# Kernel optimization log

Measured on AMD Instinct MI355X. Metric: run time of the kernel, lower is better.

Reference implementation:

```python
import jax, jax.numpy as jnp
import numpy as np
import math

DT = 1024
HID = 512
B, M, N = 16, 1024, 1024
NEG_INF = -1.0e9


def _linear(x, w, b):
    # torch nn.Linear convention: w is (out, in)
    return x @ w.T + b


def setup_inputs() -> dict:
    key = jax.random.key(0)
    ks = jax.random.split(key, 20)
    s = 0.02
    inp = {
        "oV": jax.random.normal(ks[0], (B, M, DT), jnp.float32),
        "oT": jax.random.normal(ks[1], (B, N, DT), jnp.float32),
        "Wq_v_w": jax.random.normal(ks[2], (DT, DT), jnp.float32) * s,
        "Wq_v_b": jnp.zeros((DT,), jnp.float32),
        "Wk_t_w": jax.random.normal(ks[3], (DT, DT), jnp.float32) * s,
        "Wk_t_b": jnp.zeros((DT,), jnp.float32),
        "Wv_t_w": jax.random.normal(ks[4], (DT, DT), jnp.float32) * s,
        "Wv_t_b": jnp.zeros((DT,), jnp.float32),
        "Wq_t_w": jax.random.normal(ks[5], (DT, DT), jnp.float32) * s,
        "Wq_t_b": jnp.zeros((DT,), jnp.float32),
        "Wk_v_w": jax.random.normal(ks[6], (DT, DT), jnp.float32) * s,
        "Wk_v_b": jnp.zeros((DT,), jnp.float32),
        "Wv_v_w": jax.random.normal(ks[7], (DT, DT), jnp.float32) * s,
        "Wv_v_b": jnp.zeros((DT,), jnp.float32),
        "ffn1_w": jax.random.normal(ks[8], (HID, 2 * DT), jnp.float32) * s,
        "ffn1_b": jnp.zeros((HID,), jnp.float32),
        "ffn2_w": jax.random.normal(ks[9], (1, HID), jnp.float32) * s,
        "ffn2_b": jnp.zeros((1,), jnp.float32),
    }
    return inp


def reference(oV, oT, Wq_v_w, Wq_v_b, Wk_t_w, Wk_t_b, Wv_t_w, Wv_t_b,
              Wq_t_w, Wq_t_b, Wk_v_w, Wk_v_b, Wv_v_w, Wv_v_b,
              ffn1_w, ffn1_b, ffn2_w, ffn2_b):
    dt = oV.shape[-1]
    inv_sqrt = 1.0 / math.sqrt(dt)

    # shared similarity-derived mask
    sim_raw = jnp.einsum('bmd,bnd->bmn', oV, oT)            # (B, m, n)
    v_pool = oV.mean(axis=1)                                  # (B, dt)
    t_pool = oT.mean(axis=1)                                  # (B, dt)
    h = jax.nn.relu(_linear(jnp.concatenate([v_pool, t_pool], axis=-1), ffn1_w, ffn1_b))
    l = jax.nn.sigmoid(_linear(h, ffn2_w, ffn2_b))[:, 0]      # (B,)
    S = jax.nn.softmax(sim_raw * inv_sqrt, axis=-1)
    Mmask = S >= l[:, None, None]                             # (B, m, n) bool

    # V -> T masked cross-attention
    Q_v = _linear(oV, Wq_v_w, Wq_v_b)
    K_t = _linear(oT, Wk_t_w, Wk_t_b)
    V_t = _linear(oT, Wv_t_w, Wv_t_b)
    scores_vt = jnp.einsum('bmd,bnd->bmn', Q_v, K_t) * inv_sqrt
    attn_vt = jax.nn.softmax(jnp.where(Mmask, scores_vt, NEG_INF), axis=-1)
    out_vt = jnp.einsum('bmn,bnd->bmd', attn_vt, V_t)

    # T -> V masked cross-attention (transposed mask)
    Q_t = _linear(oT, Wq_t_w, Wq_t_b)
    K_v = _linear(oV, Wk_v_w, Wk_v_b)
    V_v = _linear(oV, Wv_v_w, Wv_v_b)
    scores_tv = jnp.einsum('bnd,bmd->bnm', Q_t, K_v) * inv_sqrt
    attn_tv = jax.nn.softmax(jnp.where(Mmask.transpose(0, 2, 1), scores_tv, NEG_INF), axis=-1)
    out_tv = jnp.einsum('bnm,bmd->bnd', attn_tv, V_v)

    return out_vt, out_tv, Mmask.astype(jnp.float32)
```

## Files before the change

### kernel.cpp

```cpp
#include <hip/hip_runtime.h>
#include <stdint.h>

typedef unsigned short u16;
typedef unsigned char  u8;
typedef unsigned int   u32;
typedef unsigned long long u64;
typedef __attribute__((ext_vector_type(8))) short  short8;
typedef __attribute__((ext_vector_type(4))) float  floatx4;

#define Bz   16
#define Mm   1024
#define Nn   1024
#define Dd   1024
#define HIDh 512
#define INV_SQRT_D 0.03125f
#define NEGINF (-1.0e9f)
#define BMDc  ((size_t)Bz * Mm * Dd)
#define sMDc  ((long)Mm * Dd)

__device__ __forceinline__ float bf2f(u16 h) {
    union { u32 u; float f; } c; c.u = ((u32)h) << 16; return c.f;
}
__device__ __forceinline__ u16 f2bf(float f) {
    union { float f; u32 u; } c; c.f = f;
    u32 u = c.u;
    return (u16)((u + 0x7FFFu + ((u >> 16) & 1u)) >> 16);
}
__device__ __forceinline__ void g2lds16(const u16* g, u16* l) {
    __builtin_amdgcn_global_load_lds((const __attribute__((address_space(1))) void*)g,
                                     (__attribute__((address_space(3))) void*)l, 16, 0, 0);
}

__device__ __forceinline__ float waveSum(float v) {
#pragma unroll
    for (int o = 32; o > 0; o >>= 1) v += __shfl_xor(v, o);
    return v;
}
__device__ __forceinline__ float waveMax(float v) {
#pragma unroll
    for (int o = 32; o > 0; o >>= 1) v = fmaxf(v, __shfl_xor(v, o));
    return v;
}

template <bool OUT_FP32>
__global__ __launch_bounds__(512, 2) void gemm256(
    const u16* __restrict__ A, const u16* __restrict__ Bm,
    void* __restrict__ Cv, int K, int ldc, long sA, long sB, long sC)
{
    __shared__ __align__(16) u16 lds[2][2][256 * 64];
    const int tid  = threadIdx.x;
    const int lane = tid & 63;
    const int wv   = tid >> 6;
    const int wr   = wv >> 2;
    const int wc   = wv & 3;
    const int fr   = lane & 15, fq = lane >> 4;

    const int gX = gridDim.x, gY = gridDim.y;
    int bid = blockIdx.x + gX * (blockIdx.y + gY * blockIdx.z);
    const int nwg = gX * gY * gridDim.z;
    int wg = (bid & 7) * (nwg >> 3) + (bid >> 3);
    const int bx = wg % gX; wg /= gX;
    const int by = wg % gY;
    const int bz = wg / gY;

    const long tileM = (long)bx * 256, tileN = (long)by * 256;
    A  += (long)bz * sA;
    Bm += (long)bz * sB;
    const int T = K >> 6;

    floatx4 acc[8][4];
#pragma unroll
    for (int i = 0; i < 8; ++i)
#pragma unroll
        for (int j = 0; j < 4; ++j) acc[i][j] = (floatx4){0.f, 0.f, 0.f, 0.f};

    const int lrow = lane >> 3;
    const int scol = ((lane & 7) ^ lrow) << 3;
    const int sw   = fr & 7;
    const int kc0  = ((fq ^ sw) << 3);
    const int kc1  = (((4 + fq) ^ sw) << 3);

    auto stage = [&](int tt, int side, int hh, int bb) {
#pragma unroll
        for (int i = 0; i < 2; ++i) {
            const int j = i * 8 + wv;
            const int prow = side ? (((j >> 2) << 6) + (hh << 5) + ((j & 3) << 3))
                                  : (((j >> 3) << 7) + (hh << 6) + ((j & 7) << 3));
            const u16* src = side ? Bm : A;
            const long rb  = side ? tileN : tileM;
            g2lds16(src + (size_t)(rb + prow + lrow) * (size_t)K + (size_t)(tt << 6) + scol,
                    &lds[bb][side][prow * 64]);
        }
    };

    short8 Af[4][2], Bf[4][2];
    auto quad = [&](int mb, int nb) {
#pragma unroll
        for (int m = 0; m < 4; ++m)
#pragma unroll
            for (int n = 0; n < 2; ++n) {
                acc[mb + m][nb + n] = __builtin_amdgcn_mfma_f32_16x16x32_bf16(
                    Af[m][0], Bf[nb + n][0], acc[mb + m][nb + n], 0, 0, 0);
                acc[mb + m][nb + n] = __builtin_amdgcn_mfma_f32_16x16x32_bf16(
                    Af[m][1], Bf[nb + n][1], acc[mb + m][nb + n], 0, 0, 0);
            }
    };

    stage(0, 0, 0, 0); stage(0, 1, 0, 0); stage(0, 1, 1, 0); stage(0, 0, 1, 0);
    stage(1, 0, 0, 1); stage(1, 1, 1, 1); stage(1, 0, 1, 1);
    asm volatile("s_waitcnt vmcnt(6)" ::: "memory");
    __builtin_amdgcn_s_barrier();

    for (int t = 0; t < T; ++t) {
        const int cb = t & 1;
        const u16* lA = &lds[cb][0][0];
        const u16* lB = &lds[cb][1][0];

#pragma unroll
        for (int m = 0; m < 4; ++m) {
            const int ro = ((wr << 7) + (m << 4) + fr) * 64;
            Af[m][0] = *(const short8*)&lA[ro + kc0];
            Af[m][1] = *(const short8*)&lA[ro + kc1];
        }
#pragma unroll
        for (int n = 0; n < 2; ++n) {
            const int ro = ((wc << 6) + (n << 4) + fr) * 64;
            Bf[n][0] = *(const short8*)&lB[ro + kc0];
            Bf[n][1] = *(const short8*)&lB[ro + kc1];
        }
        if (t + 1 < T) stage(t + 1, 1, 0, cb ^ 1);
        asm volatile("" ::: "memory");
        __builtin_amdgcn_s_barrier();
        asm volatile("s_waitcnt lgkmcnt(0)" ::: "memory");
        __builtin_amdgcn_sched_barrier(0);
        __builtin_amdgcn_s_setprio(1);
        quad(0, 0);
        __builtin_amdgcn_s_setprio(0);
        asm volatile("" ::: "memory");
        __builtin_amdgcn_s_barrier();

#pragma unroll
        for (int n = 2; n < 4; ++n) {
            const int ro = ((wc << 6) + (n << 4) + fr) * 64;
            Bf[n][0] = *(const short8*)&lB[ro + kc0];
            Bf[n][1] = *(const short8*)&lB[ro + kc1];
        }
        if (t + 2 < T) stage(t + 2, 0, 0, cb);
        asm volatile("" ::: "memory");
        __builtin_amdgcn_s_barrier();
        asm volatile("s_waitcnt lgkmcnt(0)" ::: "memory");
        __builtin_amdgcn_sched_barrier(0);
        __builtin_amdgcn_s_setprio(1);
        quad(0, 2);
        __builtin_amdgcn_s_setprio(0);
        asm volatile("" ::: "memory");
        __builtin_amdgcn_s_barrier();

#pragma unroll
        for (int m = 0; m < 4; ++m) {
            const int ro = ((wr << 7) + ((m + 4) << 4) + fr) * 64;
            Af[m][0] = *(const short8*)&lA[ro + kc0];
            Af[m][1] = *(const short8*)&lA[ro + kc1];
        }
        if (t + 2 < T) stage(t + 2, 1, 1, cb);
        asm volatile("" ::: "memory");
        __builtin_amdgcn_s_barrier();
        asm volatile("s_waitcnt lgkmcnt(0)" ::: "memory");
        __builtin_amdgcn_sched_barrier(0);
        __builtin_amdgcn_s_setprio(1);
        quad(4, 2);
        __builtin_amdgcn_s_setprio(0);
        asm volatile("" ::: "memory");
        __builtin_amdgcn_s_barrier();

        if (t + 2 < T) stage(t + 2, 0, 1, cb);
        asm volatile("" ::: "memory");
        __builtin_amdgcn_s_barrier();
        __builtin_amdgcn_s_setprio(1);
        quad(4, 0);
        __builtin_amdgcn_s_setprio(0);
        if (t + 1 < T) {
            if (t + 2 < T) asm volatile("s_waitcnt vmcnt(6)" ::: "memory");
            else           asm volatile("s_waitcnt vmcnt(0)" ::: "memory");
        }
        asm volatile("" ::: "memory");
        __builtin_amdgcn_s_barrier();
    }

    __syncthreads();
    if constexpr (!OUT_FP32) {
        u16* l2 = (u16*)&lds[0][0][0];
#pragma unroll
        for (int j = 0; j < 4; ++j) {
            const int col = (wc << 6) + (j << 4) + fr;
#pragma unroll
            for (int i = 0; i < 8; ++i) {
                const int row0 = (wr << 7) + (i << 4) + (fq << 2);
#pragma unroll
                for (int r = 0; r < 4; ++r)
                    l2[(row0 + r) * 256 + col] = f2bf(acc[i][j][r]);
            }
        }
        __syncthreads();
        u16* C = (u16*)Cv + (long)bz * sC;
#pragma unroll
        for (int it = 0; it < 16; ++it) {
            const int row = it * 16 + (tid >> 5);
            const int ch  = tid & 31;
            const short8 v = *(const short8*)&l2[row * 256 + ch * 8];
            *(short8*)&C[(tileM + row) * (long)ldc + tileN + ch * 8] = v;
        }
    } else {
        float* l2f = (float*)&lds[0][0][0];
        float* C = (float*)Cv + (long)bz * sC;
#pragma unroll
        for (int pass = 0; pass < 2; ++pass) {
            if (pass) __syncthreads();
            if (wr == pass) {
#pragma unroll
                for (int j = 0; j < 4; ++j) {
                    const int col = (wc << 6) + (j << 4) + fr;
#pragma unroll
                    for (int i = 0; i < 8; ++i) {
                        const int row0 = (i << 4) + (fq << 2);
#pragma unroll
                        for (int r = 0; r < 4; ++r)
                            l2f[(row0 + r) * 256 + col] = acc[i][j][r];
                    }
                }
            }
            __syncthreads();
#pragma unroll
            for (int it = 0; it < 16; ++it) {
                const int row = it * 8 + (tid >> 6);
                const int ch  = tid & 63;
                const float4 v = *(const float4*)&l2f[row * 256 + ch * 4];
                *(float4*)&C[(tileM + pass * 128 + row) * (long)ldc + tileN + ch * 4] = v;
            }
        }
    }
}

__global__ __launch_bounds__(512, 2) void gemm_proj3(
    const u16* __restrict__ A, const u16* __restrict__ Bm,
    const float* __restrict__ bcat,
    u16* __restrict__ Pq, u16* __restrict__ Pk, u16* __restrict__ Pv, int K)
{
    __shared__ __align__(16) u16 lds[2][2][256 * 64];
    const int tid  = threadIdx.x;
    const int lane = tid & 63;
    const int wv   = tid >> 6;
    const int wr   = wv >> 2;
    const int wc   = wv & 3;
    const int fr   = lane & 15, fq = lane >> 4;

    const int bid = blockIdx.x + 64 * blockIdx.y;
    const int x  = bid & 7, l = bid >> 3;
    const int x0 = (x & 3) * 16, y0 = (x >> 2) * 6;
    const int w = l >> 5, r = l & 31;
    int bx, by;
    if (w == 0)      { bx = x0 + (r & 7);      by = y0 + (r >> 3); }
    else if (w == 1) { bx = x0 + 8 + (r & 7);  by = y0 + (r >> 3); }
    else             { bx = x0 + (r & 15);     by = y0 + 4 + (r >> 4); }

    const long tileM = (long)bx * 256, tileN = (long)by * 256;
    const int T = K >> 6;

    floatx4 acc[8][4];
#pragma unroll
    for (int i = 0; i < 8; ++i)
#pragma unroll
        for (int j = 0; j < 4; ++j) acc[i][j] = (floatx4){0.f, 0.f, 0.f, 0.f};

    const int lrow = lane >> 3;
    const int scol = ((lane & 7) ^ lrow) << 3;
    const int sw   = fr & 7;
    const int kc0  = ((fq ^ sw) << 3);
    const int kc1  = (((4 + fq) ^ sw) << 3);

    auto stage = [&](int tt, int side, int hh, int bb) {
#pragma unroll
        for (int i = 0; i < 2; ++i) {
            const int j = i * 8 + wv;
            const int prow = side ? (((j >> 2) << 6) + (hh << 5) + ((j & 3) << 3))
                                  : (((j >> 3) << 7) + (hh << 6) + ((j & 7) << 3));
            const u16* src = side ? Bm : A;
            const long rb  = side ? tileN : tileM;
            g2lds16(src + (size_t)(rb + prow + lrow) * (size_t)K + (size_t)(tt << 6) + scol,
                    &lds[bb][side][prow * 64]);
        }
    };

    short8 Af[4][2], Bf[4][2];
    auto quad = [&](int mb, int nb) {
#pragma unroll
        for (int m = 0; m < 4; ++m)
#pragma unroll
            for (int n = 0; n < 2; ++n) {
                acc[mb + m][nb + n] = __builtin_amdgcn_mfma_f32_16x16x32_bf16(
                    Af[m][0], Bf[nb + n][0], acc[mb + m][nb + n], 0, 0, 0);
                acc[mb + m][nb + n] = __builtin_amdgcn_mfma_f32_16x16x32_bf16(
                    Af[m][1], Bf[nb + n][1], acc[mb + m][nb + n], 0, 0, 0);
            }
    };

    stage(0, 0, 0, 0); stage(0, 1, 0, 0); stage(0, 1, 1, 0); stage(0, 0, 1, 0);
    stage(1, 0, 0, 1); stage(1, 1, 1, 1); stage(1, 0, 1, 1);
    asm volatile("s_waitcnt vmcnt(6)" ::: "memory");
    __builtin_amdgcn_s_barrier();

    for (int t = 0; t < T; ++t) {
        const int cb = t & 1;
        const u16* lA = &lds[cb][0][0];
        const u16* lB = &lds[cb][1][0];

#pragma unroll
        for (int m = 0; m < 4; ++m) {
            const int ro = ((wr << 7) + (m << 4) + fr) * 64;
            Af[m][0] = *(const short8*)&lA[ro + kc0];
            Af[m][1] = *(const short8*)&lA[ro + kc1];
        }
#pragma unroll
        for (int n = 0; n < 2; ++n) {
            const int ro = ((wc << 6) + (n << 4) + fr) * 64;
            Bf[n][0] = *(const short8*)&lB[ro + kc0];
            Bf[n][1] = *(const short8*)&lB[ro + kc1];
        }
        if (t + 1 < T) stage(t + 1, 1, 0, cb ^ 1);
        asm volatile("" ::: "memory");
        __builtin_amdgcn_s_barrier();
        asm volatile("s_waitcnt lgkmcnt(0)" ::: "memory");
        __builtin_amdgcn_sched_barrier(0);
        __builtin_amdgcn_s_setprio(1);
        quad(0, 0);
        __builtin_amdgcn_s_setprio(0);
        asm volatile("" ::: "memory");
        __builtin_amdgcn_s_barrier();

#pragma unroll
        for (int n = 2; n < 4; ++n) {
            const int ro = ((wc << 6) + (n << 4) + fr) * 64;
            Bf[n][0] = *(const short8*)&lB[ro + kc0];
            Bf[n][1] = *(const short8*)&lB[ro + kc1];
        }
        if (t + 2 < T) stage(t + 2, 0, 0, cb);
        asm volatile("" ::: "memory");
        __builtin_amdgcn_s_barrier();
        asm volatile("s_waitcnt lgkmcnt(0)" ::: "memory");
        __builtin_amdgcn_sched_barrier(0);
        __builtin_amdgcn_s_setprio(1);
        quad(0, 2);
        __builtin_amdgcn_s_setprio(0);
        asm volatile("" ::: "memory");
        __builtin_amdgcn_s_barrier();

#pragma unroll
        for (int m = 0; m < 4; ++m) {
            const int ro = ((wr << 7) + ((m + 4) << 4) + fr) * 64;
            Af[m][0] = *(const short8*)&lA[ro + kc0];
            Af[m][1] = *(const short8*)&lA[ro + kc1];
        }
        if (t + 2 < T) stage(t + 2, 1, 1, cb);
        asm volatile("" ::: "memory");
        __builtin_amdgcn_s_barrier();
        asm volatile("s_waitcnt lgkmcnt(0)" ::: "memory");
        __builtin_amdgcn_sched_barrier(0);
        __builtin_amdgcn_s_setprio(1);
        quad(4, 2);
        __builtin_amdgcn_s_setprio(0);
        asm volatile("" ::: "memory");
        __builtin_amdgcn_s_barrier();

        if (t + 2 < T) stage(t + 2, 0, 1, cb);
        asm volatile("" ::: "memory");
        __builtin_amdgcn_s_barrier();
        __builtin_amdgcn_s_setprio(1);
        quad(4, 0);
        __builtin_amdgcn_s_setprio(0);
        if (t + 1 < T) {
            if (t + 2 < T) asm volatile("s_waitcnt vmcnt(6)" ::: "memory");
            else           asm volatile("s_waitcnt vmcnt(0)" ::: "memory");
        }
        asm volatile("" ::: "memory");
        __builtin_amdgcn_s_barrier();
    }

    const int oid = (int)(tileN >> 10);
    __syncthreads();
    if (oid < 2) {
        u16* l2 = (u16*)&lds[0][0][0];
#pragma unroll
        for (int j = 0; j < 4; ++j) {
            const int col = (wc << 6) + (j << 4) + fr;
            const float bv = bcat[tileN + col];
#pragma unroll
            for (int i = 0; i < 8; ++i) {
                const int row0 = (wr << 7) + (i << 4) + (fq << 2);
#pragma unroll
                for (int r = 0; r < 4; ++r)
                    l2[(row0 + r) * 256 + col] = f2bf(acc[i][j][r] + bv);
            }
        }
        __syncthreads();
        u16* P = oid ? Pk : Pq;
        const long colN = tileN & 1023;
#pragma unroll
        for (int it = 0; it < 16; ++it) {
            const int row = it * 16 + (tid >> 5);
            const int ch  = tid & 31;
            const short8 v = *(const short8*)&l2[row * 256 + ch * 8];
            *(short8*)&P[(tileM + row) * (long)Dd + colN + ch * 8] = v;
        }
    } else {
        char* l2c = (char*)&lds[0][0][0];
#pragma unroll
        for (int j = 0; j < 4; ++j) {
            const int col = (wc << 6) + (j << 4) + fr;
            const float bv = bcat[tileN + col];
            const int swz = (col & 7) << 4;
#pragma unroll
            for (int i = 0; i < 8; ++i) {
                const int row0 = (wr << 7) + (i << 4) + (fq << 2);
                const u64 pk = (u64)f2bf(acc[i][j][0] + bv)
                             | ((u64)f2bf(acc[i][j][1] + bv) << 16)
                             | ((u64)f2bf(acc[i][j][2] + bv) << 32)
                             | ((u64)f2bf(acc[i][j][3] + bv) << 48);
                *(u64*)(l2c + col * 512 + ((row0 * 2) ^ swz)) = pk;
            }
        }
        __syncthreads();
        const long b  = tileM >> 10, tm = tileM & 1023;
        const long colN = tileN & 1023;
#pragma unroll
        for (int it = 0; it < 16; ++it) {
            const int col = it * 16 + (tid >> 5);
            const int ch  = tid & 31;
            const short8 v = *(const short8*)(l2c + col * 512 + ((ch * 16) ^ ((col & 7) << 4)));
            *(short8*)&Pv[b * sMDc + (colN + col) * (long)Mm + tm + ch * 8] = v;
        }
    }
}

__global__ __launch_bounds__(256) void conv_pool(
    const float* __restrict__ oV, const float* __restrict__ oT,
    u16* __restrict__ oVb, u16* __restrict__ oTb,
    float* __restrict__ vpool, float* __restrict__ tpool)
{
    const int b = blockIdx.y, srci = blockIdx.z;
    const float* src = (srci ? oT : oV) + (size_t)b * Mm * Dd;
    u16* dst = (srci ? oTb : oVb) + (size_t)b * Mm * Dd;
    const int c4 = threadIdx.x * 4;
    const int r0 = blockIdx.x * 64;
    float4 s = {0.f, 0.f, 0.f, 0.f};
    for (int r = r0; r < r0 + 64; ++r) {
        const float4 v = *(const float4*)&src[(size_t)r * Dd + c4];
        s.x += v.x; s.y += v.y; s.z += v.z; s.w += v.w;
        ushort4 o;
        o.x = f2bf(v.x); o.y = f2bf(v.y); o.z = f2bf(v.z); o.w = f2bf(v.w);
        *(ushort4*)&dst[(size_t)r * Dd + c4] = o;
    }
    float* pool = (srci ? tpool : vpool) + (size_t)b * Dd + c4;
    atomicAdd(pool + 0, s.x * (1.0f / Mm));
    atomicAdd(pool + 1, s.y * (1.0f / Mm));
    atomicAdd(pool + 2, s.z * (1.0f / Mm));
    atomicAdd(pool + 3, s.w * (1.0f / Mm));
}

__global__ __launch_bounds__(256) void wconv6(
    const float* __restrict__ w0, const float* __restrict__ w1, const float* __restrict__ w2,
    const float* __restrict__ w3, const float* __restrict__ w4, const float* __restrict__ w5,
    u16* __restrict__ dst)
{
    const float* src;
    switch (blockIdx.y) {
        case 0: src = w0; break; case 1: src = w1; break; case 2: src = w2; break;
        case 3: src = w3; break; case 4: src = w4; break; default: src = w5; break;
    }
    const size_t i = (size_t)blockIdx.x * 256 + threadIdx.x;
    const float4 a = ((const float4*)src)[2 * i];
    const float4 b = ((const float4*)src)[2 * i + 1];
    short8 o;
    o[0]=(short)f2bf(a.x); o[1]=(short)f2bf(a.y); o[2]=(short)f2bf(a.z); o[3]=(short)f2bf(a.w);
    o[4]=(short)f2bf(b.x); o[5]=(short)f2bf(b.y); o[6]=(short)f2bf(b.z); o[7]=(short)f2bf(b.w);
    *(short8*)(dst + (((size_t)blockIdx.y) << 20) + 8 * i) = o;
}

__global__ __launch_bounds__(256) void bcat_kernel(
    const float* __restrict__ b0, const float* __restrict__ b1, const float* __restrict__ b2,
    const float* __restrict__ b3, const float* __restrict__ b4, const float* __restrict__ b5,
    float* __restrict__ out)
{
    const int i = blockIdx.x * 256 + threadIdx.x;
    const int seg = i >> 10;
    const float* s;
    switch (seg) {
        case 0: s = b0; break; case 1: s = b1; break; case 2: s = b2; break;
        case 3: s = b3; break; case 4: s = b4; break; default: s = b5; break;
    }
    out[i] = s[i & 1023];
}

__global__ __launch_bounds__(256) void ffn1_kernel(
    const float* __restrict__ vpool, const float* __restrict__ tpool,
    const float* __restrict__ f1w, const float* __restrict__ f1b,
    float* __restrict__ hbuf)
{
    const int j = blockIdx.x, b = blockIdx.y;
    const int t = threadIdx.x, wv = t >> 6, lane = t & 63;
    __shared__ float red[4];
    const float* w = f1w + (size_t)j * (2 * Dd);
    float a = 0.f;
    for (int k = t; k < Dd; k += 256) a += vpool[b * Dd + k] * w[k];
    for (int k = t; k < Dd; k += 256) a += tpool[b * Dd + k] * w[Dd + k];
    a = waveSum(a);
    if (lane == 0) red[wv] = a;
    __syncthreads();
    if (t == 0) hbuf[b * HIDh + j] = fmaxf(red[0] + red[1] + red[2] + red[3] + f1b[j], 0.0f);
}

__global__ __launch_bounds__(256) void ffn2_kernel(
    const float* __restrict__ hbuf, const float* __restrict__ f2w,
    const float* __restrict__ f2b, float* __restrict__ lbuf)
{
    const int b = blockIdx.x;
    const int t = threadIdx.x, wv = t >> 6, lane = t & 63;
    __shared__ float red[4];
    float p = 0.f;
    for (int j = t; j < HIDh; j += 256) p += hbuf[b * HIDh + j] * f2w[j];
    p = waveSum(p);
    if (lane == 0) red[wv] = p;
    __syncthreads();
    if (t == 0) {
        const float z = red[0] + red[1] + red[2] + red[3] + f2b[0];
        lbuf[b] = 1.0f / (1.0f + expf(-z));
    }
}

__global__ __launch_bounds__(256) void sim_softmax_mask(
    const u16* __restrict__ scores, const float* __restrict__ lbuf, float* __restrict__ maskF)
{
    const int row = blockIdx.x, b = blockIdx.y;
    const int t = threadIdx.x, wv = t >> 6, lane = t & 63;
    __shared__ float red[8];
    const size_t off = ((size_t)b * Mm + row) * Nn;
    const uint2 sv = *(const uint2*)(scores + off + 4 * t);
    const float x0 = bf2f((u16)(sv.x & 0xFFFFu)) * INV_SQRT_D;
    const float x1 = bf2f((u16)(sv.x >> 16))     * INV_SQRT_D;
    const float x2 = bf2f((u16)(sv.y & 0xFFFFu)) * INV_SQRT_D;
    const float x3 = bf2f((u16)(sv.y >> 16))     * INV_SQRT_D;
    float mx = waveMax(fmaxf(fmaxf(x0, x1), fmaxf(x2, x3)));
    if (lane == 0) red[wv] = mx;
    __syncthreads();
    mx = fmaxf(fmaxf(red[0], red[1]), fmaxf(red[2], red[3]));
    const float e0 = expf(x0 - mx), e1 = expf(x1 - mx), e2 = expf(x2 - mx), e3 = expf(x3 - mx);
    float s = waveSum(e0 + e1 + e2 + e3);
    if (lane == 0) red[4 + wv] = s;
    __syncthreads();
    const float inv = 1.0f / fmaxf(red[4] + red[5] + red[6] + red[7], 1e-30f);
    const float l = lbuf[b];
    float4 mk;
    mk.x = (e0 * inv >= l) ? 1.0f : 0.0f;
    mk.y = (e1 * inv >= l) ? 1.0f : 0.0f;
    mk.z = (e2 * inv >= l) ? 1.0f : 0.0f;
    mk.w = (e3 * inv >= l) ? 1.0f : 0.0f;
    *(float4*)(maskF + off + 4 * t) = mk;
}

__global__ __launch_bounds__(256) void transpose_mask(
    const float* __restrict__ maskF, u8* __restrict__ maskT)
{
    __shared__ u8 tile[64][68];
    const int m0 = blockIdx.x * 64, n0 = blockIdx.y * 64, b = blockIdx.z;
    const int t = threadIdx.x;
    const int r = t >> 2, c = (t & 3) * 16;
    const float* src = maskF + ((size_t)b * Mm + (m0 + r)) * Nn + n0 + c;
    float4 f0 = ((const float4*)src)[0];
    float4 f1 = ((const float4*)src)[1];
    float4 f2 = ((const float4*)src)[2];
    float4 f3 = ((const float4*)src)[3];
    u8* dst = &tile[r][c];
    dst[0]=f0.x!=0.f; dst[1]=f0.y!=0.f; dst[2]=f0.z!=0.f; dst[3]=f0.w!=0.f;
    dst[4]=f1.x!=0.f; dst[5]=f1.y!=0.f; dst[6]=f1.z!=0.f; dst[7]=f1.w!=0.f;
    dst[8]=f2.x!=0.f; dst[9]=f2.y!=0.f; dst[10]=f2.z!=0.f; dst[11]=f2.w!=0.f;
    dst[12]=f3.x!=0.f; dst[13]=f3.y!=0.f; dst[14]=f3.z!=0.f; dst[15]=f3.w!=0.f;
    __syncthreads();
    union { u8 b[16]; uint4 v; } pk;
#pragma unroll
    for (int k = 0; k < 16; ++k) pk.b[k] = tile[c + k][r];
    *(uint4*)(maskT + ((size_t)b * Nn + (n0 + r)) * Mm + m0 + c) = pk.v;
}

template <bool TRANSP>
__global__ __launch_bounds__(256) void masked_softmax(
    u16* __restrict__ scores, const float* __restrict__ maskF, const u8* __restrict__ maskT)
{
    const int row = blockIdx.x, b = blockIdx.y;
    const int t = threadIdx.x, wv = t >> 6, lane = t & 63;
    __shared__ float red[8];
    const size_t off = ((size_t)b * Mm + row) * Nn;
    const uint2 sv = *(const uint2*)(scores + off + 4 * t);
    float x0 = bf2f((u16)(sv.x & 0xFFFFu)) * INV_SQRT_D;
    float x1 = bf2f((u16)(sv.x >> 16))     * INV_SQRT_D;
    float x2 = bf2f((u16)(sv.y & 0xFFFFu)) * INV_SQRT_D;
    float x3 = bf2f((u16)(sv.y >> 16))     * INV_SQRT_D;
    if (TRANSP) {
        const u32 mk = *(const u32*)(maskT + off + 4 * t);
        if (!(mk & 0x000000FFu)) x0 = NEGINF;
        if (!(mk & 0x0000FF00u)) x1 = NEGINF;
        if (!(mk & 0x00FF0000u)) x2 = NEGINF;
        if (!(mk & 0xFF000000u)) x3 = NEGINF;
    } else {
        const float4 mk = *(const float4*)(maskF + off + 4 * t);
        if (mk.x == 0.f) x0 = NEGINF;
        if (mk.y == 0.f) x1 = NEGINF;
        if (mk.z == 0.f) x2 = NEGINF;
        if (mk.w == 0.f) x3 = NEGINF;
    }
    float mx = waveMax(fmaxf(fmaxf(x0, x1), fmaxf(x2, x3)));
    if (lane == 0) red[wv] = mx;
    __syncthreads();
    mx = fmaxf(fmaxf(red[0], red[1]), fmaxf(red[2], red[3]));
    const float e0 = expf(x0 - mx), e1 = expf(x1 - mx), e2 = expf(x2 - mx), e3 = expf(x3 - mx);
    float s = waveSum(e0 + e1 + e2 + e3);
    if (lane == 0) red[4 + wv] = s;
    __syncthreads();
    const float inv = 1.0f / fmaxf(red[4] + red[5] + red[6] + red[7], 1e-30f);
    uint2 pk;
    pk.x = (u32)f2bf(e0 * inv) | ((u32)f2bf(e1 * inv) << 16);
    pk.y = (u32)f2bf(e2 * inv) | ((u32)f2bf(e3 * inv) << 16);
    *(uint2*)(scores + off + 4 * t) = pk;
}

extern "C" void kernel_launch(void* const* d_in, const int* in_sizes, int n_in,
                              void* d_out, int out_size, void* d_ws, size_t ws_size,
                              hipStream_t stream)
{
    (void)in_sizes; (void)n_in; (void)out_size; (void)ws_size;
    const float* oV     = (const float*)d_in[0];
    const float* oT     = (const float*)d_in[1];
    const float* Wq_v_w = (const float*)d_in[2];
    const float* Wq_v_b = (const float*)d_in[3];
    const float* Wk_t_w = (const float*)d_in[4];
    const float* Wk_t_b = (const float*)d_in[5];
    const float* Wv_t_w = (const float*)d_in[6];
    const float* Wv_t_b = (const float*)d_in[7];
    const float* Wq_t_w = (const float*)d_in[8];
    const float* Wq_t_b = (const float*)d_in[9];
    const float* Wk_v_w = (const float*)d_in[10];
    const float* Wk_v_b = (const float*)d_in[11];
    const float* Wv_v_w = (const float*)d_in[12];
    const float* Wv_v_b = (const float*)d_in[13];
    const float* f1w    = (const float*)d_in[14];
    const float* f1b    = (const float*)d_in[15];
    const float* f2w    = (const float*)d_in[16];
    const float* f2b    = (const float*)d_in[17];

    float* out_vt = (float*)d_out;
    float* out_tv = out_vt + BMDc;
    float* maskF  = out_vt + 2 * BMDc;

    u16* S0a = (u16*)d_ws;
    u16* S1a = S0a + BMDc;
    u16* S2a = S1a + BMDc;
    u16* S0b = S2a + BMDc;
    u16* S1b = S0b + BMDc;
    u16* S2b = S1b + BMDc;
    u16* S3  = S2b + BMDc;
    u16* oVb = S3 + BMDc;
    u16* oTb = oVb + BMDc;
    u16* Wc  = oTb + BMDc;
    u8*  maskT = (u8*)(Wc + 6 * (1 << 20));
    float* bcat  = (float*)(maskT + BMDc);
    float* vpool = bcat + 6144;
    float* tpool = vpool + Bz * Dd;
    float* hbuf  = tpool + Bz * Dd;
    float* lbuf  = hbuf + Bz * HIDh;

    const dim3 blk(256), blk512(512);
    const dim3 gBat(Mm / 256, Nn / 256, Bz);
    const dim3 gFproj(64, 12, 1);
    const dim3 gRow(Mm, Bz);
    const dim3 gTrp(Mm / 64, Nn / 64, Bz);
    const long sMD = sMDc, sMN = (long)Mm * Nn;

    wconv6<<<dim3(512, 6), blk, 0, stream>>>(Wq_v_w, Wk_v_w, Wv_v_w, Wq_t_w, Wk_t_w, Wv_t_w, Wc);
    bcat_kernel<<<dim3(24), blk, 0, stream>>>(Wq_v_b, Wk_v_b, Wv_v_b, Wq_t_b, Wk_t_b, Wv_t_b, bcat);

    hipMemsetAsync(vpool, 0, 2 * Bz * Dd * sizeof(float), stream);
    conv_pool<<<dim3(16, Bz, 2), blk, 0, stream>>>(oV, oT, oVb, oTb, vpool, tpool);
    ffn1_kernel<<<dim3(HIDh, Bz), blk, 0, stream>>>(vpool, tpool, f1w, f1b, hbuf);
    ffn2_kernel<<<dim3(Bz), blk, 0, stream>>>(hbuf, f2w, f2b, lbuf);

    gemm256<false><<<gBat, blk512, 0, stream>>>(oVb, oTb, S3, Dd, Nn, sMD, sMD, sMN);
    sim_softmax_mask<<<gRow, blk, 0, stream>>>(S3, lbuf, maskF);
    transpose_mask<<<gTrp, blk, 0, stream>>>(maskF, maskT);

    gemm_proj3<<<gFproj, blk512, 0, stream>>>(oVb, Wc,                 bcat,        S0a, S1b, S2b, Dd);
    gemm_proj3<<<gFproj, blk512, 0, stream>>>(oTb, Wc + 3 * (1 << 20), bcat + 3072, S0b, S1a, S2a, Dd);

    gemm256<false><<<gBat, blk512, 0, stream>>>(S0a, S1a, S3, Dd, Nn, sMD, sMD, sMN);
    masked_softmax<false><<<gRow, blk, 0, stream>>>(S3, maskF, maskT);
    gemm256<true ><<<gBat, blk512, 0, stream>>>(S3, S2a, out_vt, Nn, Dd, sMN, sMD, sMD);

    gemm256<false><<<gBat, blk512, 0, stream>>>(S0b, S1b, S3, Dd, Nn, sMD, sMD, sMN);
    masked_softmax<true><<<gRow, blk, 0, stream>>>(S3, maskF, maskT);
    gemm256<true ><<<gBat, blk512, 0, stream>>>(S3, S2b, out_tv, Nn, Dd, sMN, sMD, sMD);
}
```

Before: 826.7 us.

## Batch paired GEMMs and softmaxes into single launches, swizzle epilogue LDS, use byte mask

```diff
diff --git a/kernel.cpp b/kernel.cpp
--- a/kernel.cpp
+++ b/kernel.cpp
@@ -44,8 +44,9 @@
 
 template <bool OUT_FP32>
 __global__ __launch_bounds__(512, 2) void gemm256(
-    const u16* __restrict__ A, const u16* __restrict__ Bm,
-    void* __restrict__ Cv, int K, int ldc, long sA, long sB, long sC)
+    const u16* __restrict__ Aa, const u16* __restrict__ Ba, void* __restrict__ Ca,
+    const u16* __restrict__ Ab, const u16* __restrict__ Bb, void* __restrict__ Cb,
+    int K, int ldc, long sA, long sB, long sC)
 {
     __shared__ __align__(16) u16 lds[2][2][256 * 64];
     const int tid  = threadIdx.x;
@@ -61,11 +62,15 @@
     int wg = (bid & 7) * (nwg >> 3) + (bid >> 3);
     const int bx = wg % gX; wg /= gX;
     const int by = wg % gY;
-    const int bz = wg / gY;
+    const int bz2 = wg / gY;
+    const int br = bz2 >> 4;
+    const int bz = bz2 & 15;
+
+    const u16* A  = (br ? Ab : Aa) + (long)bz * sA;
+    const u16* Bm = (br ? Bb : Ba) + (long)bz * sB;
+    void* Cv = br ? Cb : Ca;
 
     const long tileM = (long)bx * 256, tileN = (long)by * 256;
-    A  += (long)bz * sA;
-    Bm += (long)bz * sB;
     const int T = K >> 6;
 
     floatx4 acc[8][4];
@@ -193,12 +198,15 @@
 #pragma unroll
         for (int j = 0; j < 4; ++j) {
             const int col = (wc << 6) + (j << 4) + fr;
+            const int c   = col >> 3;
 #pragma unroll
             for (int i = 0; i < 8; ++i) {
                 const int row0 = (wr << 7) + (i << 4) + (fq << 2);
 #pragma unroll
-                for (int r = 0; r < 4; ++r)
-                    l2[(row0 + r) * 256 + col] = f2bf(acc[i][j][r]);
+                for (int r = 0; r < 4; ++r) {
+                    const int row = row0 + r;
+                    l2[row * 256 + (((c + row) & 31) << 3) + (col & 7)] = f2bf(acc[i][j][r]);
+                }
             }
         }
         __syncthreads();
@@ -207,7 +215,7 @@
         for (int it = 0; it < 16; ++it) {
             const int row = it * 16 + (tid >> 5);
             const int ch  = tid & 31;
-            const short8 v = *(const short8*)&l2[row * 256 + ch * 8];
+            const short8 v = *(const short8*)&l2[row * 256 + (((ch + row) & 31) << 3)];
             *(short8*)&C[(tileM + row) * (long)ldc + tileN + ch * 8] = v;
         }
     } else {
@@ -220,12 +228,13 @@
 #pragma unroll
                 for (int j = 0; j < 4; ++j) {
                     const int col = (wc << 6) + (j << 4) + fr;
+                    const int c   = col >> 2;
 #pragma unroll
                     for (int i = 0; i < 8; ++i) {
                         const int row0 = (i << 4) + (fq << 2);
 #pragma unroll
                         for (int r = 0; r < 4; ++r)
-                            l2f[(row0 + r) * 256 + col] = acc[i][j][r];
+                            l2f[(row0 + r) * 256 + (((c + (fq << 2)) & 63) << 2) + (col & 3)] = acc[i][j][r];
                     }
                 }
             }
@@ -234,7 +243,8 @@
             for (int it = 0; it < 16; ++it) {
                 const int row = it * 8 + (tid >> 6);
                 const int ch  = tid & 63;
-                const float4 v = *(const float4*)&l2f[row * 256 + ch * 4];
+                const int rot = (row >> 2) & 3;
+                const float4 v = *(const float4*)&l2f[row * 256 + (((ch + (rot << 2)) & 63) << 2)];
                 *(float4*)&C[(tileM + pass * 128 + row) * (long)ldc + tileN + ch * 4] = v;
             }
         }
@@ -242,9 +252,10 @@
 }
 
 __global__ __launch_bounds__(512, 2) void gemm_proj3(
-    const u16* __restrict__ A, const u16* __restrict__ Bm,
-    const float* __restrict__ bcat,
-    u16* __restrict__ Pq, u16* __restrict__ Pk, u16* __restrict__ Pv, int K)
+    const u16* __restrict__ A0, const u16* __restrict__ A1,
+    const u16* __restrict__ Wcat, const float* __restrict__ bc,
+    u16* __restrict__ Pq0, u16* __restrict__ Pk0, u16* __restrict__ Pv0,
+    u16* __restrict__ Pq1, u16* __restrict__ Pk1, u16* __restrict__ Pv1, int K)
 {
     __shared__ __align__(16) u16 lds[2][2][256 * 64];
     const int tid  = threadIdx.x;
@@ -253,6 +264,14 @@
     const int wr   = wv >> 2;
     const int wc   = wv & 3;
     const int fr   = lane & 15, fq = lane >> 4;
+
+    const int z = blockIdx.z;
+    const u16* A  = z ? A1 : A0;
+    const u16* Bm = Wcat + ((size_t)z * 3 * Dd * Dd);
+    const float* bcat = bc + z * 3072;
+    u16* Pq = z ? Pq1 : Pq0;
+    u16* Pk = z ? Pk1 : Pk0;
+    u16* Pv = z ? Pv1 : Pv0;
 
     const int bid = blockIdx.x + 64 * blockIdx.y;
     const int x  = bid & 7, l = bid >> 3;
@@ -392,13 +411,16 @@
 #pragma unroll
         for (int j = 0; j < 4; ++j) {
             const int col = (wc << 6) + (j << 4) + fr;
+            const int c   = col >> 3;
             const float bv = bcat[tileN + col];
 #pragma unroll
             for (int i = 0; i < 8; ++i) {
                 const int row0 = (wr << 7) + (i << 4) + (fq << 2);
 #pragma unroll
-                for (int r = 0; r < 4; ++r)
-                    l2[(row0 + r) * 256 + col] = f2bf(acc[i][j][r] + bv);
+                for (int r = 0; r < 4; ++r) {
+                    const int row = row0 + r;
+                    l2[row * 256 + (((c + row) & 31) << 3) + (col & 7)] = f2bf(acc[i][j][r] + bv);
+                }
             }
         }
         __syncthreads();
@@ -408,7 +430,7 @@
         for (int it = 0; it < 16; ++it) {
             const int row = it * 16 + (tid >> 5);
             const int ch  = tid & 31;
-            const short8 v = *(const short8*)&l2[row * 256 + ch * 8];
+            const short8 v = *(const short8*)&l2[row * 256 + (((ch + row) & 31) << 3)];
             *(short8*)&P[(tileM + row) * (long)Dd + colN + ch * 8] = v;
         }
     } else {
@@ -537,7 +559,8 @@
 }
 
 __global__ __launch_bounds__(256) void sim_softmax_mask(
-    const u16* __restrict__ scores, const float* __restrict__ lbuf, float* __restrict__ maskF)
+    const u16* __restrict__ scores, const float* __restrict__ lbuf,
+    float* __restrict__ maskF, u8* __restrict__ maskR)
 {
     const int row = blockIdx.x, b = blockIdx.y;
     const int t = threadIdx.x, wv = t >> 6, lane = t & 63;
@@ -564,25 +587,20 @@
     mk.z = (e2 * inv >= l) ? 1.0f : 0.0f;
     mk.w = (e3 * inv >= l) ? 1.0f : 0.0f;
     *(float4*)(maskF + off + 4 * t) = mk;
+    const u32 u8mk = (mk.x != 0.f ? 1u : 0u) | (mk.y != 0.f ? 0x100u : 0u)
+                   | (mk.z != 0.f ? 0x10000u : 0u) | (mk.w != 0.f ? 0x1000000u : 0u);
+    *(u32*)(maskR + off + 4 * t) = u8mk;
 }
 
 __global__ __launch_bounds__(256) void transpose_mask(
-    const float* __restrict__ maskF, u8* __restrict__ maskT)
+    const u8* __restrict__ maskR, u8* __restrict__ maskT)
 {
     __shared__ u8 tile[64][68];
     const int m0 = blockIdx.x * 64, n0 = blockIdx.y * 64, b = blockIdx.z;
     const int t = threadIdx.x;
     const int r = t >> 2, c = (t & 3) * 16;
-    const float* src = maskF + ((size_t)b * Mm + (m0 + r)) * Nn + n0 + c;
-    float4 f0 = ((const float4*)src)[0];
-    float4 f1 = ((const float4*)src)[1];
-    float4 f2 = ((const float4*)src)[2];
-    float4 f3 = ((const float4*)src)[3];
-    u8* dst = &tile[r][c];
-    dst[0]=f0.x!=0.f; dst[1]=f0.y!=0.f; dst[2]=f0.z!=0.f; dst[3]=f0.w!=0.f;
-    dst[4]=f1.x!=0.f; dst[5]=f1.y!=0.f; dst[6]=f1.z!=0.f; dst[7]=f1.w!=0.f;
-    dst[8]=f2.x!=0.f; dst[9]=f2.y!=0.f; dst[10]=f2.z!=0.f; dst[11]=f2.w!=0.f;
-    dst[12]=f3.x!=0.f; dst[13]=f3.y!=0.f; dst[14]=f3.z!=0.f; dst[15]=f3.w!=0.f;
+    const uint4 src = *(const uint4*)(maskR + ((size_t)b * Mm + (m0 + r)) * Nn + n0 + c);
+    *(uint4*)&tile[r][c] = src;
     __syncthreads();
     union { u8 b[16]; uint4 v; } pk;
 #pragma unroll
@@ -590,11 +608,14 @@
     *(uint4*)(maskT + ((size_t)b * Nn + (n0 + r)) * Mm + m0 + c) = pk.v;
 }
 
-template <bool TRANSP>
-__global__ __launch_bounds__(256) void masked_softmax(
-    u16* __restrict__ scores, const float* __restrict__ maskF, const u8* __restrict__ maskT)
-{
-    const int row = blockIdx.x, b = blockIdx.y;
+__global__ __launch_bounds__(256) void masked_softmax2(
+    u16* __restrict__ Sa, u16* __restrict__ Sb,
+    const u8* __restrict__ mR, const u8* __restrict__ mT)
+{
+    const int row = blockIdx.x, bb = blockIdx.y;
+    const int br = bb >> 4, b = bb & 15;
+    u16* scores = br ? Sb : Sa;
+    const u8* mask = br ? mT : mR;
     const int t = threadIdx.x, wv = t >> 6, lane = t & 63;
     __shared__ float red[8];
     const size_t off = ((size_t)b * Mm + row) * Nn;
@@ -603,19 +624,11 @@
     float x1 = bf2f((u16)(sv.x >> 16))     * INV_SQRT_D;
     float x2 = bf2f((u16)(sv.y & 0xFFFFu)) * INV_SQRT_D;
     float x3 = bf2f((u16)(sv.y >> 16))     * INV_SQRT_D;
-    if (TRANSP) {
-        const u32 mk = *(const u32*)(maskT + off + 4 * t);
-        if (!(mk & 0x000000FFu)) x0 = NEGINF;
-        if (!(mk & 0x0000FF00u)) x1 = NEGINF;
-        if (!(mk & 0x00FF0000u)) x2 = NEGINF;
-        if (!(mk & 0xFF000000u)) x3 = NEGINF;
-    } else {
-        const float4 mk = *(const float4*)(maskF + off + 4 * t);
-        if (mk.x == 0.f) x0 = NEGINF;
-        if (mk.y == 0.f) x1 = NEGINF;
-        if (mk.z == 0.f) x2 = NEGINF;
-        if (mk.w == 0.f) x3 = NEGINF;
-    }
+    const u32 mk = *(const u32*)(mask + off + 4 * t);
+    if (!(mk & 0x000000FFu)) x0 = NEGINF;
+    if (!(mk & 0x0000FF00u)) x1 = NEGINF;
+    if (!(mk & 0x00FF0000u)) x2 = NEGINF;
+    if (!(mk & 0xFF000000u)) x3 = NEGINF;
     float mx = waveMax(fmaxf(fmaxf(x0, x1), fmaxf(x2, x3)));
     if (lane == 0) red[wv] = mx;
     __syncthreads();
@@ -665,12 +678,14 @@
     u16* S0b = S2a + BMDc;
     u16* S1b = S0b + BMDc;
     u16* S2b = S1b + BMDc;
-    u16* S3  = S2b + BMDc;
-    u16* oVb = S3 + BMDc;
+    u16* S3a = S2b + BMDc;
+    u16* S3b = S3a + BMDc;
+    u16* oVb = S3b + BMDc;
     u16* oTb = oVb + BMDc;
     u16* Wc  = oTb + BMDc;
     u8*  maskT = (u8*)(Wc + 6 * (1 << 20));
-    float* bcat  = (float*)(maskT + BMDc);
+    u8*  maskR = maskT + BMDc;
+    float* bcat  = (float*)(maskR + BMDc);
     float* vpool = bcat + 6144;
     float* tpool = vpool + Bz * Dd;
     float* hbuf  = tpool + Bz * Dd;
@@ -678,8 +693,9 @@
 
     const dim3 blk(256), blk512(512);
     const dim3 gBat(Mm / 256, Nn / 256, Bz);
-    const dim3 gFproj(64, 12, 1);
-    const dim3 gRow(Mm, Bz);
+    const dim3 gBat2(Mm / 256, Nn / 256, 2 * Bz);
+    const dim3 gFproj(64, 12, 2);
+    const dim3 gRow2(Mm, 2 * Bz);
     const dim3 gTrp(Mm / 64, Nn / 64, Bz);
     const long sMD = sMDc, sMN = (long)Mm * Nn;
 
@@ -691,18 +707,16 @@
     ffn1_kernel<<<dim3(HIDh, Bz), blk, 0, stream>>>(vpool, tpool, f1w, f1b, hbuf);
     ffn2_kernel<<<dim3(Bz), blk, 0, stream>>>(hbuf, f2w, f2b, lbuf);
 
-    gemm256<false><<<gBat, blk512, 0, stream>>>(oVb, oTb, S3, Dd, Nn, sMD, sMD, sMN);
-    sim_softmax_mask<<<gRow, blk, 0, stream>>>(S3, lbuf, maskF);
-    transpose_mask<<<gTrp, blk, 0, stream>>>(maskF, maskT);
-
-    gemm_proj3<<<gFproj, blk512, 0, stream>>>(oVb, Wc,                 bcat,        S0a, S1b, S2b, Dd);
-    gemm_proj3<<<gFproj, blk512, 0, stream>>>(oTb, Wc + 3 * (1 << 20), bcat + 3072, S0b, S1a, S2a, Dd);
-
-    gemm256<false><<<gBat, blk512, 0, stream>>>(S0a, S1a, S3, Dd, Nn, sMD, sMD, sMN);
-    masked_softmax<false><<<gRow, blk, 0, stream>>>(S3, maskF, maskT);
-    gemm256<true ><<<gBat, blk512, 0, stream>>>(S3, S2a, out_vt, Nn, Dd, sMN, sMD, sMD);
-
-    gemm256<false><<<gBat, blk512, 0, stream>>>(S0b, S1b, S3, Dd, Nn, sMD, sMD, sMN);
-    masked_softmax<true><<<gRow, blk, 0, stream>>>(S3, maskF, maskT);
-    gemm256<true ><<<gBat, blk512, 0, stream>>>(S3, S2b, out_tv, Nn, Dd, sMN, sMD, sMD);
-}
+    gemm256<false><<<gBat, blk512, 0, stream>>>(oVb, oTb, S3a, oVb, oTb, S3a, Dd, Nn, sMD, sMD, sMN);
+    sim_softmax_mask<<<dim3(Mm, Bz), blk, 0, stream>>>(S3a, lbuf, maskF, maskR);
+    transpose_mask<<<gTrp, blk, 0, stream>>>(maskR, maskT);
+
+    gemm_proj3<<<gFproj, blk512, 0, stream>>>(oVb, oTb, Wc, bcat,
+                                              S0a, S1b, S2b, S0b, S1a, S2a, Dd);
+
+    gemm256<false><<<gBat2, blk512, 0, stream>>>(S0a, S1a, S3a, S0b, S1b, S3b, Dd, Nn, sMD, sMD, sMN);
+
+    masked_softmax2<<<gRow2, blk, 0, stream>>>(S3a, S3b, maskR, maskT);
+
+    gemm256<true><<<gBat2, blk512, 0, stream>>>(S3a, S2a, out_vt, S3b, S2b, out_tv, Nn, Dd, sMN, sMD, sMD);
+}
```

Result: no change. 816.8 us (-1.2%).
